# Performance work log

Hardware: AMD Instinct MI355X
Metric: run time of the kernel (lower is better)

Reference implementation:

```python
import jax, jax.numpy as jnp
import numpy as np

DIM = 1024
HEADS = 16
GROUPS = 4
DIM_HEAD = 64
INNER = HEADS * DIM_HEAD  # 1024
KV_DIM = 2 * DIM_HEAD * GROUPS  # 512
B, N = 4, 2048
EPS = 1e-6


def _layernorm(x, scale, bias, eps=EPS):
    mu = jnp.mean(x, axis=-1, keepdims=True)
    var = jnp.mean(jnp.square(x - mu), axis=-1, keepdims=True)
    return (x - mu) * jax.lax.rsqrt(var + eps) * scale + bias


def setup_inputs() -> dict:
    key = jax.random.key(0)
    ks = jax.random.split(key, 10)
    lecun = lambda k, shape: jax.random.normal(k, shape, jnp.float32) * (1.0 / np.sqrt(shape[0]))
    return {
        "x": jax.random.normal(ks[0], (B, N, DIM), jnp.float32),
        "ln_scale": jnp.ones((DIM,), jnp.float32),
        "ln_bias": jnp.zeros((DIM,), jnp.float32),
        "Wq": lecun(ks[1], (DIM, INNER)),
        "Wkv": lecun(ks[2], (DIM, KV_DIM)),
        "qn_scale": jnp.ones((DIM_HEAD,), jnp.float32),
        "qn_bias": jnp.zeros((DIM_HEAD,), jnp.float32),
        "kn_scale": jnp.ones((DIM_HEAD,), jnp.float32),
        "kn_bias": jnp.zeros((DIM_HEAD,), jnp.float32),
        "Wout": lecun(ks[3], (INNER, DIM)),
    }


def reference(x, ln_scale, ln_bias, Wq, Wkv, qn_scale, qn_bias, kn_scale, kn_bias, Wout):
    b, n, _ = x.shape
    g, hg, d = GROUPS, HEADS // GROUPS, DIM_HEAD
    scale = d ** -0.5
    xn = _layernorm(x, ln_scale, ln_bias)
    # q: (b,n,inner) -> (b,h,n,d)
    q = (xn @ Wq).reshape(b, n, HEADS, d).transpose(0, 2, 1, 3)
    kv = xn @ Wkv
    k, v = jnp.split(kv, 2, axis=-1)
    # (b,n,g*d) -> (b,g,n,d)
    k = k.reshape(b, n, g, d).transpose(0, 2, 1, 3)
    v = v.reshape(b, n, g, d).transpose(0, 2, 1, 3)
    q = _layernorm(q, qn_scale, qn_bias)
    k = _layernorm(k, kn_scale, kn_bias)
    # split heads into groups: (b, g*hg, n, d) -> (b, g, hg, n, d)
    qg = q.reshape(b, g, hg, n, d)
    dots = jnp.einsum('bghqd,bgkd->bghqk', qg, k) * scale
    attn = jax.nn.softmax(dots, axis=-1)
    out = jnp.einsum('bghqk,bgkd->bghqd', attn, v)  # (b,g,hg,n,d)
    out = out.transpose(0, 3, 1, 2, 4).reshape(b, n, g * hg * d)
    return out @ Wout
```

## Files before the change

kernel.cpp:

```cpp
#include <hip/hip_runtime.h>
#include <cstdint>
#include <cstddef>

typedef unsigned short u16;
typedef __attribute__((ext_vector_type(4))) float f32x4;
typedef __attribute__((ext_vector_type(8))) __bf16 bf16x8;
typedef __attribute__((ext_vector_type(4))) __bf16 bf16x4;
typedef __attribute__((ext_vector_type(8))) unsigned short u16x8;

#define DEV static __device__ __forceinline__

#if __has_builtin(__builtin_amdgcn_exp2f)
#define EXP2(x) __builtin_amdgcn_exp2f(x)
#else
#define EXP2(x) exp2f(x)
#endif

DEV float bf2f(u16 v) { return __uint_as_float(((unsigned)v) << 16); }
DEV u16 f2bf(float f) {
  unsigned u = __float_as_uint(f);
  return (u16)((u + 0x7FFFu + ((u >> 16) & 1u)) >> 16);
}

DEV void gl_lds16(const void* g, void* l) {
  __builtin_amdgcn_global_load_lds((const __attribute__((address_space(1))) void*)g,
                                   (__attribute__((address_space(3))) void*)l, 16, 0, 0);
}

__global__ __launch_bounds__(256) void transpose64(const float* __restrict__ in,
                                                   u16* __restrict__ out, int incols) {
  __shared__ __attribute__((aligned(16))) u16 t[64 * 72];
  const int r0 = blockIdx.x * 64, c0 = blockIdx.y * 64, tid = threadIdx.x;
#pragma unroll
  for (int i = 0; i < 2; i++) {
    int c = i * 256 + tid;
    int row = c >> 3, cc = c & 7;
    const float* src = &in[(size_t)(r0 + row) * incols + c0 + cc * 8];
    f32x4 v0 = *(const f32x4*)src;
    f32x4 v1 = *(const f32x4*)(src + 4);
    u16x8 o;
#pragma unroll
    for (int j = 0; j < 4; j++) { o[j] = f2bf(v0[j]); o[4 + j] = f2bf(v1[j]); }
    *(u16x8*)&t[row * 72 + cc * 8] = o;
  }
  __syncthreads();
#pragma unroll
  for (int i = 0; i < 2; i++) {
    int c = i * 256 + tid;
    int d = c >> 3, nc = c & 7;
    u16x8 o;
#pragma unroll
    for (int j = 0; j < 8; j++) o[j] = t[(nc * 8 + j) * 72 + d];
    *(u16x8*)&out[(size_t)(c0 + d) * 1024 + r0 + nc * 8] = o;
  }
}

__global__ __launch_bounds__(256) void ln_x(const float* __restrict__ x,
                                            const float* __restrict__ sc,
                                            const float* __restrict__ bi,
                                            u16* __restrict__ xn) {
  __shared__ float red[8];
  const int row = blockIdx.x, tid = threadIdx.x;
  const int w = tid >> 6;
  f32x4 f = *(const f32x4*)&x[(size_t)row * 1024 + tid * 4];
  float s = f[0] + f[1] + f[2] + f[3];
  float q = f[0] * f[0] + f[1] * f[1] + f[2] * f[2] + f[3] * f[3];
#pragma unroll
  for (int off = 1; off < 64; off <<= 1) {
    s += __shfl_xor(s, off);
    q += __shfl_xor(q, off);
  }
  if ((tid & 63) == 0) { red[w] = s; red[4 + w] = q; }
  __syncthreads();
  float S = red[0] + red[1] + red[2] + red[3];
  float Q = red[4] + red[5] + red[6] + red[7];
  float mu = S * (1.0f / 1024.0f);
  float var = Q * (1.0f / 1024.0f) - mu * mu;
  float rs = rsqrtf(var + 1e-6f);
  f32x4 scv = *(const f32x4*)&sc[tid * 4];
  f32x4 biv = *(const f32x4*)&bi[tid * 4];
  u16* o = xn + (size_t)row * 1024 + tid * 4;
#pragma unroll
  for (int j = 0; j < 4; j++) o[j] = f2bf((f[j] - mu) * rs * scv[j] + biv[j]);
}

template <bool F32OUT>
__global__ __launch_bounds__(256) void gemm_bt(const u16* __restrict__ A,
                                               const u16* __restrict__ Bt,
                                               void* __restrict__ Cp,
                                               int M, int N, int K) {
  __shared__ __attribute__((aligned(16))) u16 Als[128 * 64];
  __shared__ __attribute__((aligned(16))) u16 Bls[128 * 64];
  const int tid = threadIdx.x;
  const int w = tid >> 6, lane = tid & 63, ln = lane & 15, quad = lane >> 4;
  const int m0 = blockIdx.y * 128, n0 = blockIdx.x * 128;
  const int moff = (w & 1) * 64, noff = (w >> 1) * 64;
  const f32x4 fzero = {0.f, 0.f, 0.f, 0.f};
  f32x4 acc[4][4];
#pragma unroll
  for (int i = 0; i < 4; i++)
#pragma unroll
    for (int j = 0; j < 4; j++) acc[i][j] = fzero;

  const u16* aS[4];
  const u16* bS[4];
#pragma unroll
  for (int i = 0; i < 4; i++) {
    int s = i * 256 + tid;
    int row = s >> 3, cs = (s & 7) ^ (row & 7);
    aS[i] = A + (size_t)(m0 + row) * K + cs * 8;
    bS[i] = Bt + (size_t)(n0 + row) * K + cs * 8;
  }

  for (int k0 = 0; k0 < K; k0 += 64) {
    __syncthreads();
#pragma unroll
    for (int i = 0; i < 4; i++) {
      int s = i * 256 + tid;
      gl_lds16(aS[i] + k0, &Als[s * 8]);
      gl_lds16(bS[i] + k0, &Bls[s * 8]);
    }
    __syncthreads();
#pragma unroll
    for (int kk = 0; kk < 2; kk++) {
      bf16x8 af[4], bfv[4];
#pragma unroll
      for (int mi = 0; mi < 4; mi++)
        af[mi] = *(const bf16x8*)
            &Als[(moff + mi * 16 + ln) * 64 + (((kk * 4 + quad) ^ (ln & 7)) * 8)];
#pragma unroll
      for (int ni = 0; ni < 4; ni++)
        bfv[ni] = *(const bf16x8*)
            &Bls[(noff + ni * 16 + ln) * 64 + (((kk * 4 + quad) ^ (ln & 7)) * 8)];
#pragma unroll
      for (int mi = 0; mi < 4; mi++)
#pragma unroll
        for (int ni = 0; ni < 4; ni++)
          acc[mi][ni] = __builtin_amdgcn_mfma_f32_16x16x32_bf16(af[mi], bfv[ni],
                                                                acc[mi][ni], 0, 0, 0);
    }
  }
#pragma unroll
  for (int mi = 0; mi < 4; mi++)
#pragma unroll
    for (int ni = 0; ni < 4; ni++)
#pragma unroll
      for (int r = 0; r < 4; r++) {
        size_t m = m0 + moff + mi * 16 + quad * 4 + r;
        size_t n = n0 + noff + ni * 16 + ln;
        if (F32OUT)
          ((float*)Cp)[m * N + n] = acc[mi][ni][r];
        else
          ((u16*)Cp)[m * N + n] = f2bf(acc[mi][ni][r]);
      }
}

__global__ __launch_bounds__(256) void qk_ln(const u16* __restrict__ qkv,
                                             const float* __restrict__ qs,
                                             const float* __restrict__ qb,
                                             const float* __restrict__ ks,
                                             const float* __restrict__ kb,
                                             u16* __restrict__ Q,
                                             u16* __restrict__ Kb) {
  const float SCL = 0.18033688011112042f;
  const int m = blockIdx.x;
  const int b = m >> 11, n = m & 2047;
  const int tid = threadIdx.x, w = tid >> 6, lane = tid & 63;
  const u16* rowp = qkv + (size_t)m * 1536;
  const float qsc = qs[lane], qbi = qb[lane];
  const float ksc = ks[lane], kbi = kb[lane];
#pragma unroll
  for (int i = 0; i < 4; i++) {
    int h = w * 4 + i;
    float v = bf2f(rowp[h * 64 + lane]);
    float s = v, q2 = v * v;
#pragma unroll
    for (int off = 1; off < 64; off <<= 1) {
      s += __shfl_xor(s, off);
      q2 += __shfl_xor(q2, off);
    }
    float mu = s * (1.0f / 64.0f);
    float var = q2 * (1.0f / 64.0f) - mu * mu;
    float y = ((v - mu) * rsqrtf(var + 1e-6f) * qsc + qbi) * SCL;
    Q[((size_t)(b * 16 + h) * 2048 + n) * 64 + lane] = f2bf(y);
  }
  {
    int g = w;
    float v = bf2f(rowp[1024 + g * 64 + lane]);
    float s = v, q2 = v * v;
#pragma unroll
    for (int off = 1; off < 64; off <<= 1) {
      s += __shfl_xor(s, off);
      q2 += __shfl_xor(q2, off);
    }
    float mu = s * (1.0f / 64.0f);
    float var = q2 * (1.0f / 64.0f) - mu * mu;
    float y = (v - mu) * rsqrtf(var + 1e-6f) * ksc + kbi;
    Kb[((size_t)(b * 4 + g) * 2048 + n) * 64 + lane] = f2bf(y);
  }
}

__global__ __launch_bounds__(256) void vtrans(const u16* __restrict__ qkv,
                                              u16* __restrict__ Vt) {
  __shared__ __attribute__((aligned(16))) u16 t[64 * 72];
  const int n0 = blockIdx.x * 64;
  const int bg = blockIdx.y;
  const int b = bg >> 2, g = bg & 3;
  const int tid = threadIdx.x;
  const u16* src = qkv + (size_t)(b * 2048 + n0) * 1536 + 1280 + g * 64;
#pragma unroll
  for (int i = 0; i < 2; i++) {
    int c = i * 256 + tid;
    int row = c >> 3, cc = c & 7;
    *(f32x4*)&t[row * 72 + cc * 8] = *(const f32x4*)&src[(size_t)row * 1536 + cc * 8];
  }
  __syncthreads();
  u16* dst = Vt + (size_t)bg * 64 * 2048 + n0;
#pragma unroll
  for (int i = 0; i < 2; i++) {
    int c = i * 256 + tid;
    int d = c >> 3, nc = c & 7;
    u16x8 o;
#pragma unroll
    for (int j = 0; j < 8; j++) o[j] = t[(nc * 8 + j) * 72 + d];
    *(u16x8*)&dst[(size_t)d * 2048 + nc * 8] = o;
  }
}

__global__ __launch_bounds__(256) void attn(const u16* __restrict__ Q,
                                            const u16* __restrict__ Kb,
                                            const u16* __restrict__ Vt,
                                            u16* __restrict__ Out) {
  __shared__ __attribute__((aligned(16))) u16 Kls[64 * 64];
  __shared__ __attribute__((aligned(16))) u16 Vls[64 * 64];
  __shared__ __attribute__((aligned(16))) u16 Pls[4][32 * 64];
  const int qt = blockIdx.x;
  const int bh = blockIdx.y;
  const int b = bh >> 4, h = bh & 15, g = h >> 2;
  const int tid = threadIdx.x, w = tid >> 6, lane = tid & 63;
  const int ln = lane & 15, quad = lane >> 4;
  const u16* Qg = Q + ((size_t)(b * 16 + h) * 2048 + qt * 128 + w * 32) * 64;
  const u16* Kg = Kb + (size_t)(b * 4 + g) * 2048 * 64;
  const u16* Vg = Vt + (size_t)(b * 4 + g) * 64 * 2048;
  const f32x4 fzero = {0.f, 0.f, 0.f, 0.f};

  bf16x8 qf[2][2];
#pragma unroll
  for (int mi = 0; mi < 2; mi++)
#pragma unroll
    for (int ks2 = 0; ks2 < 2; ks2++)
      qf[mi][ks2] = *(const bf16x8*)&Qg[(size_t)(mi * 16 + ln) * 64 + ks2 * 32 + quad * 8];

  f32x4 oacc[4][2];
#pragma unroll
  for (int ni = 0; ni < 4; ni++)
#pragma unroll
    for (int mi = 0; mi < 2; mi++) oacc[ni][mi] = fzero;
  float lsum[2] = {0.f, 0.f};
  u16* Pw = &Pls[w][0];

  const int sk0 = tid, sk1 = 256 + tid;
  const int krow0 = sk0 >> 3, kcs0 = (sk0 & 7) ^ (krow0 & 7);
  const int krow1 = sk1 >> 3, kcs1 = (sk1 & 7) ^ (krow1 & 7);

  for (int kt = 0; kt < 32; kt++) {
    __syncthreads();
    gl_lds16(Kg + (size_t)(kt * 64 + krow0) * 64 + kcs0 * 8, &Kls[sk0 * 8]);
    gl_lds16(Kg + (size_t)(kt * 64 + krow1) * 64 + kcs1 * 8, &Kls[sk1 * 8]);
    gl_lds16(Vg + (size_t)krow0 * 2048 + kt * 64 + kcs0 * 8, &Vls[sk0 * 8]);
    gl_lds16(Vg + (size_t)krow1 * 2048 + kt * 64 + kcs1 * 8, &Vls[sk1 * 8]);
    __syncthreads();

    f32x4 sacc[2][4];
#pragma unroll
    for (int ni = 0; ni < 4; ni++) {
      const int krow = ni * 16 + ln;
      bf16x8 kf0 = *(const bf16x8*)&Kls[krow * 64 + ((quad ^ (ln & 7)) * 8)];
      bf16x8 kf1 = *(const bf16x8*)&Kls[krow * 64 + (((4 + quad) ^ (ln & 7)) * 8)];
#pragma unroll
      for (int mi = 0; mi < 2; mi++) {
        f32x4 tt = __builtin_amdgcn_mfma_f32_16x16x32_bf16(kf0, qf[mi][0], fzero, 0, 0, 0);
        sacc[mi][ni] = __builtin_amdgcn_mfma_f32_16x16x32_bf16(kf1, qf[mi][1], tt, 0, 0, 0);
      }
    }

#pragma unroll
    for (int mi = 0; mi < 2; mi++) {
      float ls = 0.f;
      const int mrow = mi * 16 + ln;
#pragma unroll
      for (int ni = 0; ni < 4; ni++) {
        float p0 = EXP2(sacc[mi][ni][0]);
        float p1 = EXP2(sacc[mi][ni][1]);
        float p2 = EXP2(sacc[mi][ni][2]);
        float p3 = EXP2(sacc[mi][ni][3]);
        ls += (p0 + p1) + (p2 + p3);
        bf16x4 pv = {(__bf16)p0, (__bf16)p1, (__bf16)p2, (__bf16)p3};
        char* dst = (char*)&Pw[mrow * 64] +
                    (((2 * ni + (quad >> 1)) ^ (ln & 7)) * 16) + ((quad & 1) * 8);
        *(bf16x4*)dst = pv;
      }
      ls += __shfl_xor(ls, 16);
      ls += __shfl_xor(ls, 32);
      lsum[mi] += ls;
    }

#pragma unroll
    for (int kc = 0; kc < 2; kc++) {
      bf16x8 pf[2];
#pragma unroll
      for (int mi = 0; mi < 2; mi++)
        pf[mi] = *(const bf16x8*)
            &Pw[(mi * 16 + ln) * 64 + (((4 * kc + quad) ^ (ln & 7)) * 8)];
#pragma unroll
      for (int ni = 0; ni < 4; ni++) {
        const int drow = ni * 16 + ln;
        bf16x8 vf = *(const bf16x8*)&Vls[drow * 64 + (((4 * kc + quad) ^ (ln & 7)) * 8)];
#pragma unroll
        for (int mi = 0; mi < 2; mi++)
          oacc[ni][mi] = __builtin_amdgcn_mfma_f32_16x16x32_bf16(vf, pf[mi],
                                                                 oacc[ni][mi], 0, 0, 0);
      }
    }
  }

#pragma unroll
  for (int mi = 0; mi < 2; mi++) {
    float inv = 1.0f / lsum[mi];
    u16* Og = Out + ((size_t)b * 2048 + qt * 128 + w * 32 + mi * 16 + ln) * 1024 + h * 64;
#pragma unroll
    for (int ni = 0; ni < 4; ni++) {
      bf16x4 ov = {(__bf16)(oacc[ni][mi][0] * inv), (__bf16)(oacc[ni][mi][1] * inv),
                   (__bf16)(oacc[ni][mi][2] * inv), (__bf16)(oacc[ni][mi][3] * inv)};
      *(bf16x4*)&Og[ni * 16 + quad * 4] = ov;
    }
  }
}

extern "C" void kernel_launch(void* const* d_in, const int* in_sizes, int n_in,
                              void* d_out, int out_size, void* d_ws, size_t ws_size,
                              hipStream_t stream) {
  const float* x    = (const float*)d_in[0];
  const float* lns  = (const float*)d_in[1];
  const float* lnb  = (const float*)d_in[2];
  const float* Wq   = (const float*)d_in[3];
  const float* Wkv  = (const float*)d_in[4];
  const float* qns  = (const float*)d_in[5];
  const float* qnb  = (const float*)d_in[6];
  const float* kns  = (const float*)d_in[7];
  const float* knb  = (const float*)d_in[8];
  const float* Wout = (const float*)d_in[9];
  float* out = (float*)d_out;
  char* ws = (char*)d_ws;

  const size_t o_xn  = 0;
  const size_t o_qkv = 16777216;
  const size_t o_bt  = o_qkv + 25165824;
  const size_t o_k   = o_bt + 3145728;
  const size_t o_vt  = o_k + 4194304;
  u16* xn   = (u16*)(ws + o_xn);
  u16* qkv  = (u16*)(ws + o_qkv);
  u16* bt   = (u16*)(ws + o_bt);
  u16* Kbuf = (u16*)(ws + o_k);
  u16* Vtb  = (u16*)(ws + o_vt);
  u16* Qbuf = xn;
  u16* aout = qkv;

  transpose64<<<dim3(16, 16), 256, 0, stream>>>(Wq, bt, 1024);
  transpose64<<<dim3(16, 8), 256, 0, stream>>>(Wkv, bt + 1024 * 1024, 512);
  ln_x<<<8192, 256, 0, stream>>>(x, lns, lnb, xn);
  gemm_bt<false><<<dim3(12, 64), 256, 0, stream>>>(xn, bt, qkv, 8192, 1536, 1024);
  transpose64<<<dim3(16, 16), 256, 0, stream>>>(Wout, bt, 1024);
  qk_ln<<<8192, 256, 0, stream>>>(qkv, qns, qnb, kns, knb, Qbuf, Kbuf);
  vtrans<<<dim3(32, 16), 256, 0, stream>>>(qkv, Vtb);
  attn<<<dim3(16, 64), 256, 0, stream>>>(Qbuf, Kbuf, Vtb, aout);
  gemm_bt<true><<<dim3(8, 64), 256, 0, stream>>>(aout, bt, out, 8192, 1024, 1024);

  (void)in_sizes; (void)n_in; (void)out_size; (void)ws_size;
}
```

Before: 292.5 us.

## Halve attention query tile per block and merge small pre/post kernels

The attention kernel now gives each wave 16 query rows instead of 32. This doubles the grid to 2048 blocks, shrinks the P scratch buffer, and hoists the swizzled LDS offsets out of the loop, with launch bounds requesting more resident blocks per CU. The two weight transposes are merged into one launch, and the q/k layernorm and V transpose kernels are combined into one launch with the block index deciding the role. The smaller query tile cuts registers and improves occupancy, but each K/V tile loaded into LDS is now reused by half as many queries, so global and LDS traffic for K/V doubles.

```diff
diff --git a/kernel.cpp b/kernel.cpp
--- a/kernel.cpp
+++ b/kernel.cpp
@@ -25,6 +25,41 @@
 DEV void gl_lds16(const void* g, void* l) {
   __builtin_amdgcn_global_load_lds((const __attribute__((address_space(1))) void*)g,
                                    (__attribute__((address_space(3))) void*)l, 16, 0, 0);
+}
+
+__global__ __launch_bounds__(256) void trans_qkv_w(const float* __restrict__ Wq,
+                                                   const float* __restrict__ Wkv,
+                                                   u16* __restrict__ bt) {
+  __shared__ __attribute__((aligned(16))) u16 t[64 * 72];
+  const int r0 = blockIdx.x * 64, tid = threadIdx.x;
+  const int by = blockIdx.y;
+  const float* in;
+  int incols, c0;
+  u16* out;
+  if (by < 16) { in = Wq; incols = 1024; c0 = by * 64; out = bt; }
+  else { in = Wkv; incols = 512; c0 = (by - 16) * 64; out = bt + 1024 * 1024; }
+#pragma unroll
+  for (int i = 0; i < 2; i++) {
+    int c = i * 256 + tid;
+    int row = c >> 3, cc = c & 7;
+    const float* src = &in[(size_t)(r0 + row) * incols + c0 + cc * 8];
+    f32x4 v0 = *(const f32x4*)src;
+    f32x4 v1 = *(const f32x4*)(src + 4);
+    u16x8 o;
+#pragma unroll
+    for (int j = 0; j < 4; j++) { o[j] = f2bf(v0[j]); o[4 + j] = f2bf(v1[j]); }
+    *(u16x8*)&t[row * 72 + cc * 8] = o;
+  }
+  __syncthreads();
+#pragma unroll
+  for (int i = 0; i < 2; i++) {
+    int c = i * 256 + tid;
+    int d = c >> 3, nc = c & 7;
+    u16x8 o;
+#pragma unroll
+    for (int j = 0; j < 8; j++) o[j] = t[(nc * 8 + j) * 72 + d];
+    *(u16x8*)&out[(size_t)(c0 + d) * 1024 + r0 + nc * 8] = o;
+  }
 }
 
 __global__ __launch_bounds__(256) void transpose64(const float* __restrict__ in,
@@ -155,185 +190,190 @@
       }
 }
 
-__global__ __launch_bounds__(256) void qk_ln(const u16* __restrict__ qkv,
-                                             const float* __restrict__ qs,
-                                             const float* __restrict__ qb,
-                                             const float* __restrict__ ks,
-                                             const float* __restrict__ kb,
-                                             u16* __restrict__ Q,
-                                             u16* __restrict__ Kb) {
-  const float SCL = 0.18033688011112042f;
-  const int m = blockIdx.x;
-  const int b = m >> 11, n = m & 2047;
-  const int tid = threadIdx.x, w = tid >> 6, lane = tid & 63;
-  const u16* rowp = qkv + (size_t)m * 1536;
-  const float qsc = qs[lane], qbi = qb[lane];
-  const float ksc = ks[lane], kbi = kb[lane];
-#pragma unroll
-  for (int i = 0; i < 4; i++) {
-    int h = w * 4 + i;
-    float v = bf2f(rowp[h * 64 + lane]);
-    float s = v, q2 = v * v;
-#pragma unroll
-    for (int off = 1; off < 64; off <<= 1) {
-      s += __shfl_xor(s, off);
-      q2 += __shfl_xor(q2, off);
-    }
-    float mu = s * (1.0f / 64.0f);
-    float var = q2 * (1.0f / 64.0f) - mu * mu;
-    float y = ((v - mu) * rsqrtf(var + 1e-6f) * qsc + qbi) * SCL;
-    Q[((size_t)(b * 16 + h) * 2048 + n) * 64 + lane] = f2bf(y);
-  }
-  {
-    int g = w;
-    float v = bf2f(rowp[1024 + g * 64 + lane]);
-    float s = v, q2 = v * v;
-#pragma unroll
-    for (int off = 1; off < 64; off <<= 1) {
-      s += __shfl_xor(s, off);
-      q2 += __shfl_xor(q2, off);
-    }
-    float mu = s * (1.0f / 64.0f);
-    float var = q2 * (1.0f / 64.0f) - mu * mu;
-    float y = (v - mu) * rsqrtf(var + 1e-6f) * ksc + kbi;
-    Kb[((size_t)(b * 4 + g) * 2048 + n) * 64 + lane] = f2bf(y);
-  }
-}
-
-__global__ __launch_bounds__(256) void vtrans(const u16* __restrict__ qkv,
-                                              u16* __restrict__ Vt) {
+__global__ __launch_bounds__(256) void qkv_post(const u16* __restrict__ qkv,
+                                                const float* __restrict__ qs,
+                                                const float* __restrict__ qb,
+                                                const float* __restrict__ ks,
+                                                const float* __restrict__ kb,
+                                                u16* __restrict__ Q,
+                                                u16* __restrict__ Kb,
+                                                u16* __restrict__ Vt) {
   __shared__ __attribute__((aligned(16))) u16 t[64 * 72];
-  const int n0 = blockIdx.x * 64;
-  const int bg = blockIdx.y;
-  const int b = bg >> 2, g = bg & 3;
+  const int bid = blockIdx.x;
   const int tid = threadIdx.x;
-  const u16* src = qkv + (size_t)(b * 2048 + n0) * 1536 + 1280 + g * 64;
-#pragma unroll
-  for (int i = 0; i < 2; i++) {
-    int c = i * 256 + tid;
-    int row = c >> 3, cc = c & 7;
-    *(f32x4*)&t[row * 72 + cc * 8] = *(const f32x4*)&src[(size_t)row * 1536 + cc * 8];
-  }
-  __syncthreads();
-  u16* dst = Vt + (size_t)bg * 64 * 2048 + n0;
-#pragma unroll
-  for (int i = 0; i < 2; i++) {
-    int c = i * 256 + tid;
-    int d = c >> 3, nc = c & 7;
-    u16x8 o;
-#pragma unroll
-    for (int j = 0; j < 8; j++) o[j] = t[(nc * 8 + j) * 72 + d];
-    *(u16x8*)&dst[(size_t)d * 2048 + nc * 8] = o;
-  }
-}
-
-__global__ __launch_bounds__(256) void attn(const u16* __restrict__ Q,
-                                            const u16* __restrict__ Kb,
-                                            const u16* __restrict__ Vt,
-                                            u16* __restrict__ Out) {
+  if (bid < 8192) {
+    const float SCL = 0.18033688011112042f;
+    const int b = bid >> 11, n = bid & 2047;
+    const int w = tid >> 6, lane = tid & 63;
+    const u16* rowp = qkv + (size_t)bid * 1536;
+    const float qsc = qs[lane], qbi = qb[lane];
+    const float ksc = ks[lane], kbi = kb[lane];
+#pragma unroll
+    for (int i = 0; i < 4; i++) {
+      int h = w * 4 + i;
+      float v = bf2f(rowp[h * 64 + lane]);
+      float s = v, q2 = v * v;
+#pragma unroll
+      for (int off = 1; off < 64; off <<= 1) {
+        s += __shfl_xor(s, off);
+        q2 += __shfl_xor(q2, off);
+      }
+      float mu = s * (1.0f / 64.0f);
+      float var = q2 * (1.0f / 64.0f) - mu * mu;
+      float y = ((v - mu) * rsqrtf(var + 1e-6f) * qsc + qbi) * SCL;
+      Q[((size_t)(b * 16 + h) * 2048 + n) * 64 + lane] = f2bf(y);
+    }
+    {
+      int g = w;
+      float v = bf2f(rowp[1024 + g * 64 + lane]);
+      float s = v, q2 = v * v;
+#pragma unroll
+      for (int off = 1; off < 64; off <<= 1) {
+        s += __shfl_xor(s, off);
+        q2 += __shfl_xor(q2, off);
+      }
+      float mu = s * (1.0f / 64.0f);
+      float var = q2 * (1.0f / 64.0f) - mu * mu;
+      float y = (v - mu) * rsqrtf(var + 1e-6f) * ksc + kbi;
+      Kb[((size_t)(b * 4 + g) * 2048 + n) * 64 + lane] = f2bf(y);
+    }
+  } else {
+    const int idx = bid - 8192;
+    const int n0 = (idx & 31) * 64;
+    const int bg = idx >> 5;
+    const int b = bg >> 2, g = bg & 3;
+    const u16* src = qkv + (size_t)(b * 2048 + n0) * 1536 + 1280 + g * 64;
+#pragma unroll
+    for (int i = 0; i < 2; i++) {
+      int c = i * 256 + tid;
+      int row = c >> 3, cc = c & 7;
+      *(f32x4*)&t[row * 72 + cc * 8] = *(const f32x4*)&src[(size_t)row * 1536 + cc * 8];
+    }
+    __syncthreads();
+    u16* dst = Vt + (size_t)bg * 64 * 2048 + n0;
+#pragma unroll
+    for (int i = 0; i < 2; i++) {
+      int c = i * 256 + tid;
+      int d = c >> 3, nc = c & 7;
+      u16x8 o;
+#pragma unroll
+      for (int j = 0; j < 8; j++) o[j] = t[(nc * 8 + j) * 72 + d];
+      *(u16x8*)&dst[(size_t)d * 2048 + nc * 8] = o;
+    }
+  }
+}
+
+__global__ __launch_bounds__(256, 5) void attn(const u16* __restrict__ Q,
+                                               const u16* __restrict__ Kb,
+                                               const u16* __restrict__ Vt,
+                                               u16* __restrict__ Out) {
   __shared__ __attribute__((aligned(16))) u16 Kls[64 * 64];
   __shared__ __attribute__((aligned(16))) u16 Vls[64 * 64];
-  __shared__ __attribute__((aligned(16))) u16 Pls[4][32 * 64];
+  __shared__ __attribute__((aligned(16))) u16 Pls[4][16 * 64];
   const int qt = blockIdx.x;
   const int bh = blockIdx.y;
   const int b = bh >> 4, h = bh & 15, g = h >> 2;
   const int tid = threadIdx.x, w = tid >> 6, lane = tid & 63;
   const int ln = lane & 15, quad = lane >> 4;
-  const u16* Qg = Q + ((size_t)(b * 16 + h) * 2048 + qt * 128 + w * 32) * 64;
+  const u16* Qg = Q + ((size_t)(b * 16 + h) * 2048 + qt * 64 + w * 16) * 64;
   const u16* Kg = Kb + (size_t)(b * 4 + g) * 2048 * 64;
   const u16* Vg = Vt + (size_t)(b * 4 + g) * 64 * 2048;
   const f32x4 fzero = {0.f, 0.f, 0.f, 0.f};
 
-  bf16x8 qf[2][2];
-#pragma unroll
-  for (int mi = 0; mi < 2; mi++)
-#pragma unroll
-    for (int ks2 = 0; ks2 < 2; ks2++)
-      qf[mi][ks2] = *(const bf16x8*)&Qg[(size_t)(mi * 16 + ln) * 64 + ks2 * 32 + quad * 8];
-
-  f32x4 oacc[4][2];
-#pragma unroll
-  for (int ni = 0; ni < 4; ni++)
-#pragma unroll
-    for (int mi = 0; mi < 2; mi++) oacc[ni][mi] = fzero;
-  float lsum[2] = {0.f, 0.f};
+  bf16x8 qf[2];
+#pragma unroll
+  for (int ks2 = 0; ks2 < 2; ks2++)
+    qf[ks2] = *(const bf16x8*)&Qg[(size_t)ln * 64 + ks2 * 32 + quad * 8];
+
+  f32x4 oacc[4];
+#pragma unroll
+  for (int ni = 0; ni < 4; ni++) oacc[ni] = fzero;
+  float lsum = 0.f;
   u16* Pw = &Pls[w][0];
 
   const int sk0 = tid, sk1 = 256 + tid;
   const int krow0 = sk0 >> 3, kcs0 = (sk0 & 7) ^ (krow0 & 7);
   const int krow1 = sk1 >> 3, kcs1 = (sk1 & 7) ^ (krow1 & 7);
+  const u16* kp0 = Kg + (size_t)krow0 * 64 + kcs0 * 8;
+  const u16* kp1 = Kg + (size_t)krow1 * 64 + kcs1 * 8;
+  const u16* vp0 = Vg + (size_t)krow0 * 2048 + kcs0 * 8;
+  const u16* vp1 = Vg + (size_t)krow1 * 2048 + kcs1 * 8;
+  u16* kd0 = &Kls[sk0 * 8];
+  u16* kd1 = &Kls[sk1 * 8];
+  u16* vd0 = &Vls[sk0 * 8];
+  u16* vd1 = &Vls[sk1 * 8];
+  int koffA[4], koffB[4], vroff[4][2];
+#pragma unroll
+  for (int ni = 0; ni < 4; ni++) {
+    const int row = ni * 16 + ln;
+    koffA[ni] = row * 64 + ((quad ^ (ln & 7)) * 8);
+    koffB[ni] = row * 64 + (((4 + quad) ^ (ln & 7)) * 8);
+#pragma unroll
+    for (int kc = 0; kc < 2; kc++)
+      vroff[ni][kc] = row * 64 + (((4 * kc + quad) ^ (ln & 7)) * 8);
+  }
+  char* pst[4];
+#pragma unroll
+  for (int ni = 0; ni < 4; ni++)
+    pst[ni] = (char*)Pw + ln * 128 + (((2 * ni + (quad >> 1)) ^ (ln & 7)) * 16) +
+              ((quad & 1) * 8);
+  int proff[2];
+#pragma unroll
+  for (int kc = 0; kc < 2; kc++)
+    proff[kc] = ln * 64 + (((4 * kc + quad) ^ (ln & 7)) * 8);
 
   for (int kt = 0; kt < 32; kt++) {
     __syncthreads();
-    gl_lds16(Kg + (size_t)(kt * 64 + krow0) * 64 + kcs0 * 8, &Kls[sk0 * 8]);
-    gl_lds16(Kg + (size_t)(kt * 64 + krow1) * 64 + kcs1 * 8, &Kls[sk1 * 8]);
-    gl_lds16(Vg + (size_t)krow0 * 2048 + kt * 64 + kcs0 * 8, &Vls[sk0 * 8]);
-    gl_lds16(Vg + (size_t)krow1 * 2048 + kt * 64 + kcs1 * 8, &Vls[sk1 * 8]);
+    gl_lds16(kp0, kd0);
+    gl_lds16(kp1, kd1);
+    gl_lds16(vp0, vd0);
+    gl_lds16(vp1, vd1);
+    kp0 += 64 * 64; kp1 += 64 * 64;
+    vp0 += 64; vp1 += 64;
     __syncthreads();
 
-    f32x4 sacc[2][4];
+    f32x4 sacc[4];
 #pragma unroll
     for (int ni = 0; ni < 4; ni++) {
-      const int krow = ni * 16 + ln;
-      bf16x8 kf0 = *(const bf16x8*)&Kls[krow * 64 + ((quad ^ (ln & 7)) * 8)];
-      bf16x8 kf1 = *(const bf16x8*)&Kls[krow * 64 + (((4 + quad) ^ (ln & 7)) * 8)];
-#pragma unroll
-      for (int mi = 0; mi < 2; mi++) {
-        f32x4 tt = __builtin_amdgcn_mfma_f32_16x16x32_bf16(kf0, qf[mi][0], fzero, 0, 0, 0);
-        sacc[mi][ni] = __builtin_amdgcn_mfma_f32_16x16x32_bf16(kf1, qf[mi][1], tt, 0, 0, 0);
+      bf16x8 kf0 = *(const bf16x8*)&Kls[koffA[ni]];
+      bf16x8 kf1 = *(const bf16x8*)&Kls[koffB[ni]];
+      f32x4 tt = __builtin_amdgcn_mfma_f32_16x16x32_bf16(kf0, qf[0], fzero, 0, 0, 0);
+      sacc[ni] = __builtin_amdgcn_mfma_f32_16x16x32_bf16(kf1, qf[1], tt, 0, 0, 0);
+    }
+
+    float ls = 0.f;
+#pragma unroll
+    for (int ni = 0; ni < 4; ni++) {
+      float p0 = EXP2(sacc[ni][0]);
+      float p1 = EXP2(sacc[ni][1]);
+      float p2 = EXP2(sacc[ni][2]);
+      float p3 = EXP2(sacc[ni][3]);
+      ls += (p0 + p1) + (p2 + p3);
+      bf16x4 pv = {(__bf16)p0, (__bf16)p1, (__bf16)p2, (__bf16)p3};
+      *(bf16x4*)pst[ni] = pv;
+    }
+    ls += __shfl_xor(ls, 16);
+    ls += __shfl_xor(ls, 32);
+    lsum += ls;
+
+#pragma unroll
+    for (int kc = 0; kc < 2; kc++) {
+      bf16x8 pf = *(const bf16x8*)&Pw[proff[kc]];
+#pragma unroll
+      for (int ni = 0; ni < 4; ni++) {
+        bf16x8 vf = *(const bf16x8*)&Vls[vroff[ni][kc]];
+        oacc[ni] = __builtin_amdgcn_mfma_f32_16x16x32_bf16(vf, pf, oacc[ni], 0, 0, 0);
       }
     }
-
-#pragma unroll
-    for (int mi = 0; mi < 2; mi++) {
-      float ls = 0.f;
-      const int mrow = mi * 16 + ln;
-#pragma unroll
-      for (int ni = 0; ni < 4; ni++) {
-        float p0 = EXP2(sacc[mi][ni][0]);
-        float p1 = EXP2(sacc[mi][ni][1]);
-        float p2 = EXP2(sacc[mi][ni][2]);
-        float p3 = EXP2(sacc[mi][ni][3]);
-        ls += (p0 + p1) + (p2 + p3);
-        bf16x4 pv = {(__bf16)p0, (__bf16)p1, (__bf16)p2, (__bf16)p3};
-        char* dst = (char*)&Pw[mrow * 64] +
-                    (((2 * ni + (quad >> 1)) ^ (ln & 7)) * 16) + ((quad & 1) * 8);
-        *(bf16x4*)dst = pv;
-      }
-      ls += __shfl_xor(ls, 16);
-      ls += __shfl_xor(ls, 32);
-      lsum[mi] += ls;
-    }
-
-#pragma unroll
-    for (int kc = 0; kc < 2; kc++) {
-      bf16x8 pf[2];
-#pragma unroll
-      for (int mi = 0; mi < 2; mi++)
-        pf[mi] = *(const bf16x8*)
-            &Pw[(mi * 16 + ln) * 64 + (((4 * kc + quad) ^ (ln & 7)) * 8)];
-#pragma unroll
-      for (int ni = 0; ni < 4; ni++) {
-        const int drow = ni * 16 + ln;
-        bf16x8 vf = *(const bf16x8*)&Vls[drow * 64 + (((4 * kc + quad) ^ (ln & 7)) * 8)];
-#pragma unroll
-        for (int mi = 0; mi < 2; mi++)
-          oacc[ni][mi] = __builtin_amdgcn_mfma_f32_16x16x32_bf16(vf, pf[mi],
-                                                                 oacc[ni][mi], 0, 0, 0);
-      }
-    }
-  }
-
-#pragma unroll
-  for (int mi = 0; mi < 2; mi++) {
-    float inv = 1.0f / lsum[mi];
-    u16* Og = Out + ((size_t)b * 2048 + qt * 128 + w * 32 + mi * 16 + ln) * 1024 + h * 64;
-#pragma unroll
-    for (int ni = 0; ni < 4; ni++) {
-      bf16x4 ov = {(__bf16)(oacc[ni][mi][0] * inv), (__bf16)(oacc[ni][mi][1] * inv),
-                   (__bf16)(oacc[ni][mi][2] * inv), (__bf16)(oacc[ni][mi][3] * inv)};
-      *(bf16x4*)&Og[ni * 16 + quad * 4] = ov;
-    }
+  }
+
+  const float inv = 1.0f / lsum;
+  u16* Og = Out + ((size_t)b * 2048 + qt * 64 + w * 16 + ln) * 1024 + h * 64;
+#pragma unroll
+  for (int ni = 0; ni < 4; ni++) {
+    bf16x4 ov = {(__bf16)(oacc[ni][0] * inv), (__bf16)(oacc[ni][1] * inv),
+                 (__bf16)(oacc[ni][2] * inv), (__bf16)(oacc[ni][3] * inv)};
+    *(bf16x4*)&Og[ni * 16 + quad * 4] = ov;
   }
 }
 
@@ -366,14 +406,12 @@
   u16* Qbuf = xn;
   u16* aout = qkv;
 
-  transpose64<<<dim3(16, 16), 256, 0, stream>>>(Wq, bt, 1024);
-  transpose64<<<dim3(16, 8), 256, 0, stream>>>(Wkv, bt + 1024 * 1024, 512);
+  trans_qkv_w<<<dim3(16, 24), 256, 0, stream>>>(Wq, Wkv, bt);
   ln_x<<<8192, 256, 0, stream>>>(x, lns, lnb, xn);
   gemm_bt<false><<<dim3(12, 64), 256, 0, stream>>>(xn, bt, qkv, 8192, 1536, 1024);
   transpose64<<<dim3(16, 16), 256, 0, stream>>>(Wout, bt, 1024);
-  qk_ln<<<8192, 256, 0, stream>>>(qkv, qns, qnb, kns, knb, Qbuf, Kbuf);
-  vtrans<<<dim3(32, 16), 256, 0, stream>>>(qkv, Vtb);
-  attn<<<dim3(16, 64), 256, 0, stream>>>(Qbuf, Kbuf, Vtb, aout);
+  qkv_post<<<8704, 256, 0, stream>>>(qkv, qns, qnb, kns, knb, Qbuf, Kbuf, Vtb);
+  attn<<<dim3(32, 64), 256, 0, stream>>>(Qbuf, Kbuf, Vtb, aout);
   gemm_bt<true><<<dim3(8, 64), 256, 0, stream>>>(aout, bt, out, 8192, 1024, 1024);
 
   (void)in_sizes; (void)n_in; (void)out_size; (void)ws_size;
```

Result: no change. 296.9 us (+1.5%).
